# Performance work log

Hardware: AMD Instinct MI355X
Metric: run time of the kernel (lower is better)

The kernel has to match this reference:

```python
import jax, jax.numpy as jnp
import numpy as np

EPS = 1e-5

def _act_quant(x):
    # per-token int8 absmax quantization with straight-through estimator
    scale = 127.0 / jnp.clip(jnp.max(jnp.abs(x), axis=-1, keepdims=True), EPS, None)
    q = jnp.clip(jnp.round(x * scale), -128.0, 127.0) / scale
    return x + jax.lax.stop_gradient(q - x)

def _weight_quant(w):
    # per-tensor ternary (1.58-bit) quantization with STE
    scale = 1.0 / jnp.clip(jnp.mean(jnp.abs(w)), EPS, None)
    q = jnp.clip(jnp.round(w * scale), -1.0, 1.0) / scale
    return w + jax.lax.stop_gradient(q - w)

def _bitlinear(x, w, b):
    y = jnp.einsum('bsd,od->bso', _act_quant(x), _weight_quant(w))
    return y + b

def setup_inputs() -> dict:
    key = jax.random.key(0)
    k1, k2, k3, k4, k5 = jax.random.split(key, 5)
    B, S, D, F = 8, 4096, 1024, 3072
    return {
        'x': jax.random.normal(k1, (B, S, D), dtype=jnp.float32),
        'up_w': jax.random.normal(k2, (F, D), dtype=jnp.float32) * 0.125,
        'up_b': jax.random.normal(k3, (F,), dtype=jnp.float32) * 0.01,
        'down_w': jax.random.normal(k4, (D, F), dtype=jnp.float32) * 0.125,
        'down_b': jax.random.normal(k5, (D,), dtype=jnp.float32) * 0.01,
    }

def reference(x, up_w, up_b, down_w, down_b):
    hidden = _bitlinear(x, up_w, up_b)          # [B,S,3072]
    hidden = jnp.square(jax.nn.relu(hidden))    # relu(h)^2
    return _bitlinear(hidden, down_w, down_b)   # [B,S,1024]
```

## Files before the change

### kernel.cpp

```cpp
#include <hip/hip_runtime.h>
#include <hip/hip_bf16.h>
#include <stdint.h>

#define EPS 1e-5f

typedef int v4i __attribute__((ext_vector_type(4)));
typedef int v16i __attribute__((ext_vector_type(16)));
typedef const __attribute__((address_space(1))) void g_void;
typedef __attribute__((address_space(3))) void l_void;

__device__ inline float block_max_nw(float v, int nw) {
    __shared__ float s[8];
#pragma unroll
    for (int o = 32; o; o >>= 1) v = fmaxf(v, __shfl_xor(v, o, 64));
    if ((threadIdx.x & 63) == 0) s[threadIdx.x >> 6] = v;
    __syncthreads();
    float m = s[0];
    for (int i = 1; i < nw; ++i) m = fmaxf(m, s[i]);
    return m;
}

__device__ inline float block_sum64x4(float v) {
    __shared__ float s[4];
#pragma unroll
    for (int o = 32; o; o >>= 1) v += __shfl_xor(v, o, 64);
    if ((threadIdx.x & 63) == 0) s[threadIdx.x >> 6] = v;
    __syncthreads();
    return s[0] + s[1] + s[2] + s[3];
}

__global__ __launch_bounds__(256) void abs_sum_part_k(const float4* __restrict__ w,
                                                      int n4, float* __restrict__ part) {
    float s = 0.0f;
    for (int i = blockIdx.x * 256 + threadIdx.x; i < n4; i += 1024 * 256) {
        float4 v = w[i];
        s += fabsf(v.x) + fabsf(v.y) + fabsf(v.z) + fabsf(v.w);
    }
    s = block_sum64x4(s);
    if (threadIdx.x == 0) part[blockIdx.x] = s;
}

__global__ __launch_bounds__(256) void abs_sum_final_k(const float* __restrict__ parts,
                                                       float* __restrict__ sums) {
    const float* p = parts + blockIdx.x * 1024;
    const int t = threadIdx.x;
    float s = p[t] + p[t + 256] + p[t + 512] + p[t + 768];
    s = block_sum64x4(s);
    if (t == 0) sums[blockIdx.x] = s;
}

__global__ __launch_bounds__(256) void wquant_k(const float4* __restrict__ w,
                                                char4* __restrict__ q,
                                                const float* __restrict__ sum) {
    const float mean = fmaxf(sum[0] * (1.0f / 3145728.0f), EPS);
    const float scale = 1.0f / mean;
    const int i = blockIdx.x * 256 + threadIdx.x;
    float4 v = w[i];
    char4 c;
    c.x = (signed char)(int)fmaxf(fminf(rintf(v.x * scale), 1.0f), -1.0f);
    c.y = (signed char)(int)fmaxf(fminf(rintf(v.y * scale), 1.0f), -1.0f);
    c.z = (signed char)(int)fmaxf(fminf(rintf(v.z * scale), 1.0f), -1.0f);
    c.w = (signed char)(int)fmaxf(fminf(rintf(v.w * scale), 1.0f), -1.0f);
    q[i] = c;
}

__global__ __launch_bounds__(256) void aquant_k(const float4* __restrict__ x,
                                                char4* __restrict__ q,
                                                float* __restrict__ deq) {
    const int row = blockIdx.x, t = threadIdx.x;
    const float4 v = x[(size_t)row * 256 + t];
    float m = fmaxf(fmaxf(fabsf(v.x), fabsf(v.y)), fmaxf(fabsf(v.z), fabsf(v.w)));
    m = block_max_nw(m, 4);
    const float mc = fmaxf(m, EPS);
    const float sc = 127.0f / mc;
    char4 c;
    c.x = (signed char)(int)fmaxf(fminf(rintf(v.x * sc), 127.0f), -128.0f);
    c.y = (signed char)(int)fmaxf(fminf(rintf(v.y * sc), 127.0f), -128.0f);
    c.z = (signed char)(int)fmaxf(fminf(rintf(v.z * sc), 127.0f), -128.0f);
    c.w = (signed char)(int)fmaxf(fminf(rintf(v.w * sc), 127.0f), -128.0f);
    q[(size_t)row * 256 + t] = c;
    if (t == 0) deq[row] = mc / 127.0f;
}

__global__ __launch_bounds__(384) void hquant_k(unsigned short* __restrict__ hid,
                                                float* __restrict__ deq) {
    const size_t row = blockIdx.x;
    const int t = threadIdx.x;
    unsigned short* rp = hid + row * 3072;
    const uint4 u = ((const uint4*)rp)[t];
    float v[8];
    {
        uint32_t uu[4] = {u.x, u.y, u.z, u.w};
#pragma unroll
        for (int i = 0; i < 4; ++i) {
            uint32_t lo = uu[i] << 16, hi = uu[i] & 0xFFFF0000u;
            v[2 * i]     = __uint_as_float(lo);
            v[2 * i + 1] = __uint_as_float(hi);
        }
    }
    float m = 0.0f;
#pragma unroll
    for (int i = 0; i < 8; ++i) m = fmaxf(m, fabsf(v[i]));
    m = block_max_nw(m, 6);
    const float mc = fmaxf(m, EPS);
    const float sc = 127.0f / mc;
    uint32_t p0 = 0, p1 = 0;
#pragma unroll
    for (int i = 0; i < 4; ++i) {
        int c = (int)fminf(rintf(v[i] * sc), 127.0f);
        p0 |= (uint32_t)(c & 255) << (8 * i);
    }
#pragma unroll
    for (int i = 0; i < 4; ++i) {
        int c = (int)fminf(rintf(v[4 + i] * sc), 127.0f);
        p1 |= (uint32_t)(c & 255) << (8 * i);
    }
    uint2 pk; pk.x = p0; pk.y = p1;
    ((uint2*)rp)[t] = pk;
    if (t == 0) deq[row] = mc / 127.0f;
}

template <bool RELU2, typename OutT>
__global__ __launch_bounds__(256, 2) void gemm_i8(
    const int8_t* __restrict__ A, int lda,
    const int8_t* __restrict__ B, int ldb,
    OutT* __restrict__ O, int ldo,
    const float* __restrict__ rowDeq,
    const float* __restrict__ sumPtr,
    const float* __restrict__ bias,
    int K, int nTiles) {
    __shared__ __align__(16) char lds[3][24576];
    const int t = threadIdx.x;
    const int lane = t & 63;
    const int w = t >> 6;
    const int xcd = blockIdx.x & 7;
    const int sb = blockIdx.x >> 3;
    const int bm = xcd + 8 * (sb / nTiles);
    const int bn = sb % nTiles;
    const long m0 = (long)bm * 128;
    const long n0 = (long)bn * 256;

    v16i acc[2][4];
#pragma unroll
    for (int i = 0; i < 2; ++i)
#pragma unroll
        for (int j = 0; j < 4; ++j) acc[i][j] = (v16i)(0);

    const int mloc = (w >> 1) * 64;
    const int nloc = (w & 1) * 128;
    const int r32 = lane & 31;
    const int h = lane >> 5;

    const int srow = lane >> 2;
    const int sc = ((lane & 3) ^ ((lane >> 3) & 3)) * 16;
    const int8_t* paS = A + (m0 + w * 32 + srow) * (long)lda + sc;
    const int8_t* pbS = B + (n0 + w * 64 + srow) * (long)ldb + sc;

    int cro[2];
#pragma unroll
    for (int ks = 0; ks < 2; ++ks) cro[ks] = ((2 * ks + h) ^ ((r32 >> 1) & 3)) * 16;

    const int NT = K >> 6;

    auto STAGE = [&](int tt) {
        char* buf = lds[tt % 3];
        const long ko = (long)tt << 6;
#pragma unroll
        for (int r = 0; r < 2; ++r)
            __builtin_amdgcn_global_load_lds(
                (g_void*)(paS + (long)(r * 16) * lda + ko),
                (l_void*)(buf + w * 2048 + r * 1024 + lane * 16), 16, 0, 0);
#pragma unroll
        for (int r = 0; r < 4; ++r)
            __builtin_amdgcn_global_load_lds(
                (g_void*)(pbS + (long)(r * 16) * ldb + ko),
                (l_void*)(buf + 8192 + w * 4096 + r * 1024 + lane * 16), 16, 0, 0);
    };

    STAGE(0);
    STAGE(1);
    asm volatile("s_waitcnt vmcnt(6)" ::: "memory");
    __builtin_amdgcn_s_barrier();
    __builtin_amdgcn_sched_barrier(0);

    for (int tt = 0; tt < NT; ++tt) {
        const char* buf = lds[tt % 3];
        const bool pf = (tt + 2 < NT);
        if (pf) STAGE(tt + 2);
        __builtin_amdgcn_sched_barrier(0);
#pragma unroll
        for (int ks = 0; ks < 2; ++ks) {
            v4i af[2], bf[4];
#pragma unroll
            for (int mt = 0; mt < 2; ++mt)
                af[mt] = *(const v4i*)(buf + (mloc + mt * 32 + r32) * 64 + cro[ks]);
#pragma unroll
            for (int nt = 0; nt < 4; ++nt)
                bf[nt] = *(const v4i*)(buf + 8192 + (nloc + nt * 32 + r32) * 64 + cro[ks]);
            __builtin_amdgcn_s_setprio(1);
#pragma unroll
            for (int mt = 0; mt < 2; ++mt)
#pragma unroll
                for (int nt = 0; nt < 4; ++nt)
                    acc[mt][nt] = __builtin_amdgcn_mfma_i32_32x32x32_i8(
                        af[mt], bf[nt], acc[mt][nt], 0, 0, 0);
            __builtin_amdgcn_s_setprio(0);
        }
        if (tt + 1 < NT) {
            if (pf) asm volatile("s_waitcnt vmcnt(6)" ::: "memory");
            else    asm volatile("s_waitcnt vmcnt(0)" ::: "memory");
            __builtin_amdgcn_s_barrier();
            __builtin_amdgcn_sched_barrier(0);
        }
    }

    const float wdeq = fmaxf(sumPtr[0] * (1.0f / 3145728.0f), EPS);
#pragma unroll
    for (int mt = 0; mt < 2; ++mt) {
#pragma unroll
        for (int g = 0; g < 4; ++g) {
#pragma unroll
            for (int rr = 0; rr < 4; ++rr) {
                const long row = m0 + mloc + mt * 32 + g * 8 + h * 4 + rr;
                const float rs = rowDeq[row] * wdeq;
#pragma unroll
                for (int nt = 0; nt < 4; ++nt) {
                    const long col = n0 + nloc + nt * 32 + r32;
                    float val = (float)acc[mt][nt][g * 4 + rr] * rs + bias[col];
                    if (RELU2) {
                        val = fmaxf(val, 0.0f);
                        val = val * val;
                    }
                    O[row * (long)ldo + col] = (OutT)val;
                }
            }
        }
    }
}

extern "C" void kernel_launch(void* const* d_in, const int* in_sizes, int n_in,
                              void* d_out, int out_size, void* d_ws, size_t ws_size,
                              hipStream_t stream) {
    const float* x      = (const float*)d_in[0];
    const float* up_w   = (const float*)d_in[1];
    const float* up_b   = (const float*)d_in[2];
    const float* down_w = (const float*)d_in[3];
    const float* down_b = (const float*)d_in[4];

    char* ws = (char*)d_ws;
    float*  sums   = (float*)ws;
    float*  parts  = (float*)(ws + 256);
    int8_t* qw_dn  = (int8_t*)(ws + 256 + 8192);
    float*  deqh   = (float*)(ws + 256 + 8192 + 3145728);
    __hip_bfloat16* hidden = (__hip_bfloat16*)(ws + 256 + 8192 + 3145728 + 131072);

    int8_t* qx    = (int8_t*)d_out;
    int8_t* qw_up = qx + 33554432;
    float*  deqx  = (float*)(qx + 33554432 + 3145728);

    abs_sum_part_k<<<1024, 256, 0, stream>>>((const float4*)up_w, 786432, parts);
    abs_sum_part_k<<<1024, 256, 0, stream>>>((const float4*)down_w, 786432, parts + 1024);
    abs_sum_final_k<<<2, 256, 0, stream>>>(parts, sums);

    wquant_k<<<3072, 256, 0, stream>>>((const float4*)up_w, (char4*)qw_up, &sums[0]);
    wquant_k<<<3072, 256, 0, stream>>>((const float4*)down_w, (char4*)qw_dn, &sums[1]);
    aquant_k<<<32768, 256, 0, stream>>>((const float4*)x, (char4*)qx, deqx);

    gemm_i8<true, __hip_bfloat16><<<3072, 256, 0, stream>>>(
        qx, 1024, qw_up, 1024, hidden, 3072, deqx, &sums[0], up_b, 1024, 12);
    hquant_k<<<32768, 384, 0, stream>>>((unsigned short*)hidden, deqh);
    gemm_i8<false, float><<<1024, 256, 0, stream>>>(
        (const int8_t*)hidden, 6144, qw_dn, 3072, (float*)d_out, 1024,
        deqh, &sums[1], down_b, 3072, 4);
}
```

Measured before the change: 538.0 us.

## Use wave-per-row quantization and compile-time K in int8 GEMM

The activation and hidden quantization kernels now handle one row per wavefront, four rows per block. Each uses only a warp shuffle reduction, which removes the shared-memory block reduction and its __syncthreads. The int8 GEMM takes K and the tile count as template parameters so the K loop can be fully unrolled with precomputed LDS read pointers. It also loads both k-substeps' fragments before issuing the MFMAs and drops the setprio hints. Full unrolling and hoisted fragments raise register pressure and code size, which could hurt occupancy at launch_bounds(256,2).

```diff
diff --git a/kernel.cpp b/kernel.cpp
--- a/kernel.cpp
+++ b/kernel.cpp
@@ -8,17 +8,6 @@
 typedef int v16i __attribute__((ext_vector_type(16)));
 typedef const __attribute__((address_space(1))) void g_void;
 typedef __attribute__((address_space(3))) void l_void;
-
-__device__ inline float block_max_nw(float v, int nw) {
-    __shared__ float s[8];
-#pragma unroll
-    for (int o = 32; o; o >>= 1) v = fmaxf(v, __shfl_xor(v, o, 64));
-    if ((threadIdx.x & 63) == 0) s[threadIdx.x >> 6] = v;
-    __syncthreads();
-    float m = s[0];
-    for (int i = 1; i < nw; ++i) m = fmaxf(m, s[i]);
-    return m;
-}
 
 __device__ inline float block_sum64x4(float v) {
     __shared__ float s[4];
@@ -67,76 +56,93 @@
 __global__ __launch_bounds__(256) void aquant_k(const float4* __restrict__ x,
                                                 char4* __restrict__ q,
                                                 float* __restrict__ deq) {
-    const int row = blockIdx.x, t = threadIdx.x;
-    const float4 v = x[(size_t)row * 256 + t];
-    float m = fmaxf(fmaxf(fabsf(v.x), fabsf(v.y)), fmaxf(fabsf(v.z), fabsf(v.w)));
-    m = block_max_nw(m, 4);
+    const int wv = threadIdx.x >> 6, lane = threadIdx.x & 63;
+    const size_t row = (size_t)blockIdx.x * 4 + wv;
+    const float4* xr = x + row * 256;
+    float4 v[4];
+    float m = 0.0f;
+#pragma unroll
+    for (int j = 0; j < 4; ++j) {
+        v[j] = xr[j * 64 + lane];
+        m = fmaxf(m, fmaxf(fmaxf(fabsf(v[j].x), fabsf(v[j].y)),
+                           fmaxf(fabsf(v[j].z), fabsf(v[j].w))));
+    }
+#pragma unroll
+    for (int o = 32; o; o >>= 1) m = fmaxf(m, __shfl_xor(m, o, 64));
     const float mc = fmaxf(m, EPS);
     const float sc = 127.0f / mc;
-    char4 c;
-    c.x = (signed char)(int)fmaxf(fminf(rintf(v.x * sc), 127.0f), -128.0f);
-    c.y = (signed char)(int)fmaxf(fminf(rintf(v.y * sc), 127.0f), -128.0f);
-    c.z = (signed char)(int)fmaxf(fminf(rintf(v.z * sc), 127.0f), -128.0f);
-    c.w = (signed char)(int)fmaxf(fminf(rintf(v.w * sc), 127.0f), -128.0f);
-    q[(size_t)row * 256 + t] = c;
-    if (t == 0) deq[row] = mc / 127.0f;
-}
-
-__global__ __launch_bounds__(384) void hquant_k(unsigned short* __restrict__ hid,
+    char4* qr = q + row * 256;
+#pragma unroll
+    for (int j = 0; j < 4; ++j) {
+        char4 c;
+        c.x = (signed char)(int)fmaxf(fminf(rintf(v[j].x * sc), 127.0f), -128.0f);
+        c.y = (signed char)(int)fmaxf(fminf(rintf(v[j].y * sc), 127.0f), -128.0f);
+        c.z = (signed char)(int)fmaxf(fminf(rintf(v[j].z * sc), 127.0f), -128.0f);
+        c.w = (signed char)(int)fmaxf(fminf(rintf(v[j].w * sc), 127.0f), -128.0f);
+        qr[j * 64 + lane] = c;
+    }
+    if (lane == 0) deq[row] = mc / 127.0f;
+}
+
+__global__ __launch_bounds__(256) void hquant_k(unsigned short* __restrict__ hid,
                                                 float* __restrict__ deq) {
-    const size_t row = blockIdx.x;
-    const int t = threadIdx.x;
+    const int wv = threadIdx.x >> 6, lane = threadIdx.x & 63;
+    const size_t row = (size_t)blockIdx.x * 4 + wv;
     unsigned short* rp = hid + row * 3072;
-    const uint4 u = ((const uint4*)rp)[t];
-    float v[8];
-    {
+    float vals[48];
+    float m = 0.0f;
+#pragma unroll
+    for (int j = 0; j < 6; ++j) {
+        const uint4 u = ((const uint4*)rp)[j * 64 + lane];
         uint32_t uu[4] = {u.x, u.y, u.z, u.w};
 #pragma unroll
         for (int i = 0; i < 4; ++i) {
-            uint32_t lo = uu[i] << 16, hi = uu[i] & 0xFFFF0000u;
-            v[2 * i]     = __uint_as_float(lo);
-            v[2 * i + 1] = __uint_as_float(hi);
-        }
-    }
-    float m = 0.0f;
-#pragma unroll
-    for (int i = 0; i < 8; ++i) m = fmaxf(m, fabsf(v[i]));
-    m = block_max_nw(m, 6);
+            vals[j * 8 + 2 * i]     = __uint_as_float(uu[i] << 16);
+            vals[j * 8 + 2 * i + 1] = __uint_as_float(uu[i] & 0xFFFF0000u);
+        }
+#pragma unroll
+        for (int i = 0; i < 8; ++i) m = fmaxf(m, vals[j * 8 + i]);
+    }
+#pragma unroll
+    for (int o = 32; o; o >>= 1) m = fmaxf(m, __shfl_xor(m, o, 64));
     const float mc = fmaxf(m, EPS);
     const float sc = 127.0f / mc;
-    uint32_t p0 = 0, p1 = 0;
-#pragma unroll
-    for (int i = 0; i < 4; ++i) {
-        int c = (int)fminf(rintf(v[i] * sc), 127.0f);
-        p0 |= (uint32_t)(c & 255) << (8 * i);
-    }
-#pragma unroll
-    for (int i = 0; i < 4; ++i) {
-        int c = (int)fminf(rintf(v[4 + i] * sc), 127.0f);
-        p1 |= (uint32_t)(c & 255) << (8 * i);
-    }
-    uint2 pk; pk.x = p0; pk.y = p1;
-    ((uint2*)rp)[t] = pk;
-    if (t == 0) deq[row] = mc / 127.0f;
-}
-
-template <bool RELU2, typename OutT>
+#pragma unroll
+    for (int j = 0; j < 6; ++j) {
+        uint32_t p0 = 0, p1 = 0;
+#pragma unroll
+        for (int i = 0; i < 4; ++i) {
+            int c = (int)fminf(rintf(vals[j * 8 + i] * sc), 127.0f);
+            p0 |= (uint32_t)(c & 255) << (8 * i);
+        }
+#pragma unroll
+        for (int i = 0; i < 4; ++i) {
+            int c = (int)fminf(rintf(vals[j * 8 + 4 + i] * sc), 127.0f);
+            p1 |= (uint32_t)(c & 255) << (8 * i);
+        }
+        uint2 pk; pk.x = p0; pk.y = p1;
+        ((uint2*)rp)[j * 64 + lane] = pk;
+    }
+    if (lane == 0) deq[row] = mc / 127.0f;
+}
+
+template <int K, int NTILES, bool RELU2, typename OutT>
 __global__ __launch_bounds__(256, 2) void gemm_i8(
     const int8_t* __restrict__ A, int lda,
     const int8_t* __restrict__ B, int ldb,
     OutT* __restrict__ O, int ldo,
     const float* __restrict__ rowDeq,
     const float* __restrict__ sumPtr,
-    const float* __restrict__ bias,
-    int K, int nTiles) {
+    const float* __restrict__ bias) {
+    constexpr int NT = K >> 6;
     __shared__ __align__(16) char lds[3][24576];
     const int t = threadIdx.x;
     const int lane = t & 63;
     const int w = t >> 6;
     const int xcd = blockIdx.x & 7;
     const int sb = blockIdx.x >> 3;
-    const int bm = xcd + 8 * (sb / nTiles);
-    const int bn = sb % nTiles;
+    const int bm = xcd + 8 * (sb / NTILES);
+    const int bn = sb % NTILES;
     const long m0 = (long)bm * 128;
     const long n0 = (long)bn * 256;
 
@@ -152,29 +158,35 @@
     const int h = lane >> 5;
 
     const int srow = lane >> 2;
-    const int sc = ((lane & 3) ^ ((lane >> 3) & 3)) * 16;
-    const int8_t* paS = A + (m0 + w * 32 + srow) * (long)lda + sc;
-    const int8_t* pbS = B + (n0 + w * 64 + srow) * (long)ldb + sc;
-
-    int cro[2];
-#pragma unroll
-    for (int ks = 0; ks < 2; ++ks) cro[ks] = ((2 * ks + h) ^ ((r32 >> 1) & 3)) * 16;
-
-    const int NT = K >> 6;
+    const int scS = ((lane & 3) ^ ((lane >> 3) & 3)) * 16;
+    const int8_t* paS0 = A + (m0 + w * 32 + srow) * (long)lda + scS;
+    const int8_t* paS1 = paS0 + 16 * (long)lda;
+    const int8_t* pbS0 = B + (n0 + w * 64 + srow) * (long)ldb + scS;
+    const int8_t* pbS1 = pbS0 + 16 * (long)ldb;
+    const int8_t* pbS2 = pbS0 + 32 * (long)ldb;
+    const int8_t* pbS3 = pbS0 + 48 * (long)ldb;
+
+    const int swz = (r32 >> 1) & 3;
+    const char* rdA0 = &lds[0][0] + (mloc + r32) * 64 + ((h ^ swz) * 16);
+    const char* rdA1 = &lds[0][0] + (mloc + r32) * 64 + (((2 + h) ^ swz) * 16);
+    const char* rdB0 = &lds[0][0] + 8192 + (nloc + r32) * 64 + ((h ^ swz) * 16);
+    const char* rdB1 = &lds[0][0] + 8192 + (nloc + r32) * 64 + (((2 + h) ^ swz) * 16);
 
     auto STAGE = [&](int tt) {
-        char* buf = lds[tt % 3];
+        char* buf = &lds[0][0] + (tt % 3) * 24576;
         const long ko = (long)tt << 6;
-#pragma unroll
-        for (int r = 0; r < 2; ++r)
-            __builtin_amdgcn_global_load_lds(
-                (g_void*)(paS + (long)(r * 16) * lda + ko),
-                (l_void*)(buf + w * 2048 + r * 1024 + lane * 16), 16, 0, 0);
-#pragma unroll
-        for (int r = 0; r < 4; ++r)
-            __builtin_amdgcn_global_load_lds(
-                (g_void*)(pbS + (long)(r * 16) * ldb + ko),
-                (l_void*)(buf + 8192 + w * 4096 + r * 1024 + lane * 16), 16, 0, 0);
+        __builtin_amdgcn_global_load_lds((g_void*)(paS0 + ko),
+                                         (l_void*)(buf + w * 2048), 16, 0, 0);
+        __builtin_amdgcn_global_load_lds((g_void*)(paS1 + ko),
+                                         (l_void*)(buf + w * 2048 + 1024), 16, 0, 0);
+        __builtin_amdgcn_global_load_lds((g_void*)(pbS0 + ko),
+                                         (l_void*)(buf + 8192 + w * 4096), 16, 0, 0);
+        __builtin_amdgcn_global_load_lds((g_void*)(pbS1 + ko),
+                                         (l_void*)(buf + 8192 + w * 4096 + 1024), 16, 0, 0);
+        __builtin_amdgcn_global_load_lds((g_void*)(pbS2 + ko),
+                                         (l_void*)(buf + 8192 + w * 4096 + 2048), 16, 0, 0);
+        __builtin_amdgcn_global_load_lds((g_void*)(pbS3 + ko),
+                                         (l_void*)(buf + 8192 + w * 4096 + 3072), 16, 0, 0);
     };
 
     STAGE(0);
@@ -183,32 +195,33 @@
     __builtin_amdgcn_s_barrier();
     __builtin_amdgcn_sched_barrier(0);
 
+#pragma unroll
     for (int tt = 0; tt < NT; ++tt) {
-        const char* buf = lds[tt % 3];
-        const bool pf = (tt + 2 < NT);
-        if (pf) STAGE(tt + 2);
-        __builtin_amdgcn_sched_barrier(0);
+        const int bo = (tt % 3) * 24576;
+        if (tt + 2 < NT) STAGE(tt + 2);
+        v4i af[2][2], bf[2][4];
 #pragma unroll
         for (int ks = 0; ks < 2; ++ks) {
-            v4i af[2], bf[4];
+            const char* rA = ks ? rdA1 : rdA0;
+            const char* rB = ks ? rdB1 : rdB0;
 #pragma unroll
             for (int mt = 0; mt < 2; ++mt)
-                af[mt] = *(const v4i*)(buf + (mloc + mt * 32 + r32) * 64 + cro[ks]);
+                af[ks][mt] = *(const v4i*)(rA + bo + mt * 2048);
 #pragma unroll
             for (int nt = 0; nt < 4; ++nt)
-                bf[nt] = *(const v4i*)(buf + 8192 + (nloc + nt * 32 + r32) * 64 + cro[ks]);
-            __builtin_amdgcn_s_setprio(1);
+                bf[ks][nt] = *(const v4i*)(rB + bo + nt * 2048);
+        }
+#pragma unroll
+        for (int ks = 0; ks < 2; ++ks)
 #pragma unroll
             for (int mt = 0; mt < 2; ++mt)
 #pragma unroll
                 for (int nt = 0; nt < 4; ++nt)
                     acc[mt][nt] = __builtin_amdgcn_mfma_i32_32x32x32_i8(
-                        af[mt], bf[nt], acc[mt][nt], 0, 0, 0);
-            __builtin_amdgcn_s_setprio(0);
-        }
+                        af[ks][mt], bf[ks][nt], acc[mt][nt], 0, 0, 0);
         if (tt + 1 < NT) {
-            if (pf) asm volatile("s_waitcnt vmcnt(6)" ::: "memory");
-            else    asm volatile("s_waitcnt vmcnt(0)" ::: "memory");
+            if (tt + 2 < NT) asm volatile("s_waitcnt vmcnt(6) lgkmcnt(0)" ::: "memory");
+            else             asm volatile("s_waitcnt vmcnt(0) lgkmcnt(0)" ::: "memory");
             __builtin_amdgcn_s_barrier();
             __builtin_amdgcn_sched_barrier(0);
         }
@@ -264,12 +277,12 @@
 
     wquant_k<<<3072, 256, 0, stream>>>((const float4*)up_w, (char4*)qw_up, &sums[0]);
     wquant_k<<<3072, 256, 0, stream>>>((const float4*)down_w, (char4*)qw_dn, &sums[1]);
-    aquant_k<<<32768, 256, 0, stream>>>((const float4*)x, (char4*)qx, deqx);
-
-    gemm_i8<true, __hip_bfloat16><<<3072, 256, 0, stream>>>(
-        qx, 1024, qw_up, 1024, hidden, 3072, deqx, &sums[0], up_b, 1024, 12);
-    hquant_k<<<32768, 384, 0, stream>>>((unsigned short*)hidden, deqh);
-    gemm_i8<false, float><<<1024, 256, 0, stream>>>(
+    aquant_k<<<8192, 256, 0, stream>>>((const float4*)x, (char4*)qx, deqx);
+
+    gemm_i8<1024, 12, true, __hip_bfloat16><<<3072, 256, 0, stream>>>(
+        qx, 1024, qw_up, 1024, hidden, 3072, deqx, &sums[0], up_b);
+    hquant_k<<<8192, 256, 0, stream>>>((unsigned short*)hidden, deqh);
+    gemm_i8<3072, 4, false, float><<<1024, 256, 0, stream>>>(
         (const int8_t*)hidden, 6144, qw_dn, 3072, (float*)d_out, 1024,
-        deqh, &sums[1], down_b, 3072, 4);
-}
+        deqh, &sums[1], down_b);
+}
```

Result: faster. 523.7 us (-2.7%).
